# Kernel optimization log

Hardware: AMD Instinct MI355X
Metric: run time of the kernel (lower is better)

## Reference

```python
import jax, jax.numpy as jnp
import numpy as np


def setup_inputs() -> dict:
    key = jax.random.key(0)
    ks = jax.random.split(key, 8)
    bs, G, A, C, CM, D, H = 256, 169, 3, 5, 32, 1024, 512
    return {
        "boxes_sml0": jax.random.uniform(ks[0], (bs, G, A, C), dtype=jnp.float32),
        "masks_in0": jax.random.normal(ks[1], (bs, G, A, CM), dtype=jnp.float32),
        "feat": jax.random.normal(ks[2], (bs, D, 13, 13), dtype=jnp.float32),
        "lang_feat": jax.random.normal(ks[3], (bs, H), dtype=jnp.float32),
        "W_vs": jax.random.normal(ks[4], (D, H), dtype=jnp.float32) * 0.02,
        "b_vs": jnp.zeros((H,), dtype=jnp.float32),
        "W_ts": jax.random.normal(ks[5], (H, H), dtype=jnp.float32) * 0.02,
        "b_ts": jnp.zeros((H,), dtype=jnp.float32),
        "select_num": 32,
    }


def reference(boxes_sml0, masks_in0, feat, lang_feat, W_vs, b_vs, W_ts, b_ts, select_num):
    bs, G, A, C = boxes_sml0.shape
    CM = masks_in0.shape[-1]
    D = feat.shape[1]

    # mean over anchors of objectness channel 4 -> top-k grid selection
    mean_score = jnp.mean(boxes_sml0[..., 4], axis=2)           # [bs, G]
    _, idx = jax.lax.top_k(mean_score, select_num)              # [bs, k]

    # scatter-mask + masked_select in torch == gather of selected grids
    boxes_new = jnp.take_along_axis(boxes_sml0, idx[:, :, None, None], axis=1)  # [bs,k,A,C]
    masks_new = jnp.take_along_axis(masks_in0, idx[:, :, None, None], axis=1)   # [bs,k,A,CM]

    # gather visual features of selected grids, project
    i_all = feat.reshape(bs, D, -1).transpose(0, 2, 1)          # [bs, G, D]
    i_sel = jnp.take_along_axis(i_all, idx[:, :, None], axis=1) # [bs, k, D]
    x_new = i_sel @ W_vs + b_vs                                 # [bs, k, H]
    y_new = lang_feat @ W_ts + b_ts                             # [bs, H]

    # head: visual-text similarity, pick top grid per batch
    sim = jnp.einsum('bkh,bh->bk', x_new, y_new)                # [bs, k]
    maxval = jnp.max(sim, axis=1)                               # [bs]
    pred = jnp.argmax(sim, axis=1)                              # [bs]

    sel_b = jnp.take_along_axis(boxes_new, pred[:, None, None, None], axis=1)[:, 0]  # [bs,A,C]
    sel_m = jnp.take_along_axis(masks_new, pred[:, None, None, None], axis=1)[:, 0]  # [bs,A,CM]

    # cxcywh -> xyxy with original in-place overwrite semantics
    cx, cy, w, h = sel_b[..., 0], sel_b[..., 1], sel_b[..., 2], sel_b[..., 3]
    x1 = cx - w / 2
    y1 = cy - h / 2
    x2 = x1 + w
    y2 = y1 + h
    refined = jnp.concatenate(
        [jnp.stack([x1, y1, x2, y2], axis=-1), sel_b[..., 4:]], axis=-1)  # [bs,A,C]

    # pick anchor with max objectness, gather 5-dim box and mask coeffs
    aidx = jnp.argmax(refined[..., 4], axis=1)                  # [bs]
    box_new = jnp.take_along_axis(refined[..., :5], aidx[:, None, None], axis=1)  # [bs,1,5]
    mask_new = jnp.take_along_axis(sel_m, aidx[:, None, None], axis=1)            # [bs,1,CM]
    return box_new, mask_new, maxval
```

## Files before the change

### kernel.cpp

```cpp
#include <hip/hip_runtime.h>
#include <cfloat>
#include <cstdint>

#define GBM 64
#define GBN 64
#define GBK 64
#define GPAD 68

#define G_    169
#define D_    1024
#define NW    8
#define SLAB  128
#define ROWG  8
#define NGRP  16
#define GRPF  1352
#define NV    338
#define NBUF  3
#define SPL   8

typedef unsigned int u32;

__device__ __forceinline__ void gload_lds16(const float* g, float* l) {
    __builtin_amdgcn_global_load_lds(
        (const __attribute__((address_space(1))) u32*)g,
        (__attribute__((address_space(3))) u32*)l, 16, 0, 0);
}

__device__ __forceinline__ void stage_group(const float* gsrc, float* ldsbase, int lane) {
    #pragma unroll
    for (int j = 0; j < 6; j++) {
        int idx = j * 64 + lane;
        if (idx < NV)
            gload_lds16(gsrc + 4 * idx, ldsbase + j * 256);
    }
}

__global__ __launch_bounds__(256) void gemm_splitk(
    const float* __restrict__ A, const float* __restrict__ B,
    float* __restrict__ Cpart, int M, int N, int K)
{
    __shared__ __align__(16) float Asm[GBK][GPAD];
    __shared__ __align__(16) float Bsm[GBK][GPAD];
    int t  = threadIdx.x;
    int m0 = blockIdx.y * GBM, n0 = blockIdx.x * GBN;
    int ks = blockIdx.z * GBK;

    #pragma unroll
    for (int i = 0; i < 4; i++) {
        int v = t + 256 * i;
        int m = v >> 4, k4 = (v & 15) * 4;
        float4 x = *(const float4*)&A[(size_t)(m0 + m) * K + ks + k4];
        Asm[k4 + 0][m] = x.x; Asm[k4 + 1][m] = x.y;
        Asm[k4 + 2][m] = x.z; Asm[k4 + 3][m] = x.w;
    }
    #pragma unroll
    for (int i = 0; i < 4; i++) {
        int v = t + 256 * i;
        int r = v >> 4, c4 = (v & 15) * 4;
        *(float4*)&Bsm[r][c4] = *(const float4*)&B[(size_t)(ks + r) * N + n0 + c4];
    }
    __syncthreads();

    int r4 = (t >> 4) * 4, c4 = (t & 15) * 4;
    float acc[4][4] = {{0.f}};
    #pragma unroll
    for (int kk = 0; kk < GBK; kk++) {
        float4 a = *(const float4*)&Asm[kk][r4];
        float4 b = *(const float4*)&Bsm[kk][c4];
        float av[4] = {a.x, a.y, a.z, a.w};
        float bv[4] = {b.x, b.y, b.z, b.w};
        #pragma unroll
        for (int i = 0; i < 4; i++)
            #pragma unroll
            for (int j = 0; j < 4; j++) acc[i][j] += av[i] * bv[j];
    }
    float* Cp = Cpart + (size_t)blockIdx.z * M * N;
    #pragma unroll
    for (int i = 0; i < 4; i++) {
        float4 v = {acc[i][0], acc[i][1], acc[i][2], acc[i][3]};
        *(float4*)&Cp[(size_t)(m0 + r4 + i) * N + n0 + c4] = v;
    }
}

__global__ __launch_bounds__(256) void gemm2_fused(
    const float* __restrict__ py, const float* __restrict__ b_ts,
    const float* __restrict__ W, float* __restrict__ pz,
    int M, int N, int K)
{
    __shared__ __align__(16) float Asm[GBK][GPAD];
    __shared__ __align__(16) float Bsm[GBK][GPAD];
    int t  = threadIdx.x;
    int m0 = blockIdx.y * GBM, n0 = blockIdx.x * GBN;
    int ks = blockIdx.z * GBK;

    #pragma unroll
    for (int i = 0; i < 4; i++) {
        int v = t + 256 * i;
        int m = v >> 4, h4 = (v & 15) * 4;
        float4 x = *(const float4*)&b_ts[ks + h4];
        #pragma unroll
        for (int s = 0; s < SPL; s++) {
            float4 p = *(const float4*)&py[((size_t)s * M + m0 + m) * K + ks + h4];
            x.x += p.x; x.y += p.y; x.z += p.z; x.w += p.w;
        }
        Asm[h4 + 0][m] = x.x; Asm[h4 + 1][m] = x.y;
        Asm[h4 + 2][m] = x.z; Asm[h4 + 3][m] = x.w;
    }
    #pragma unroll
    for (int i = 0; i < 4; i++) {
        int v = t + 256 * i;
        int n = v >> 4, k4 = (v & 15) * 4;
        float4 x = *(const float4*)&W[(size_t)(n0 + n) * K + ks + k4];
        Bsm[k4 + 0][n] = x.x; Bsm[k4 + 1][n] = x.y;
        Bsm[k4 + 2][n] = x.z; Bsm[k4 + 3][n] = x.w;
    }
    __syncthreads();

    int r4 = (t >> 4) * 4, c4 = (t & 15) * 4;
    float acc[4][4] = {{0.f}};
    #pragma unroll
    for (int kk = 0; kk < GBK; kk++) {
        float4 a = *(const float4*)&Asm[kk][r4];
        float4 b = *(const float4*)&Bsm[kk][c4];
        float av[4] = {a.x, a.y, a.z, a.w};
        float bv[4] = {b.x, b.y, b.z, b.w};
        #pragma unroll
        for (int i = 0; i < 4; i++)
            #pragma unroll
            for (int j = 0; j < 4; j++) acc[i][j] += av[i] * bv[j];
    }
    float* Cp = pz + (size_t)blockIdx.z * M * N;
    #pragma unroll
    for (int i = 0; i < 4; i++) {
        float4 v = {acc[i][0], acc[i][1], acc[i][2], acc[i][3]};
        *(float4*)&Cp[(size_t)(m0 + r4 + i) * N + n0 + c4] = v;
    }
}

__global__ __launch_bounds__(512) void feat_final(
    const float* __restrict__ feat, const float* __restrict__ pz,
    const float* __restrict__ boxes, const float* __restrict__ masks,
    const float* __restrict__ py, const float* __restrict__ b_ts,
    const float* __restrict__ b_vs, const int* __restrict__ kptr,
    float* __restrict__ out_box, float* __restrict__ out_mask,
    float* __restrict__ out_max,
    int bs, int AN, int CH, int CM, int H)
{
    __shared__ __align__(16) float buf[NW][NBUF][GRPF];
    __shared__ __align__(16) float zs[D_];
    __shared__ float accw[NW * 192];
    __shared__ float simall[176];
    __shared__ float ms[176];
    __shared__ int   selg[176];
    __shared__ float simv[176];
    __shared__ float redw[NW];
    __shared__ float bbs;
    __shared__ int   selp[2];

    const int b = blockIdx.x;
    const int t = threadIdx.x;
    const int w = t >> 6, lane = t & 63;

    {
        int h2 = t * 2;
        float2 s = {0.f, 0.f};
        #pragma unroll
        for (int sp = 0; sp < SPL; sp++) {
            float2 v = *(const float2*)&pz[((size_t)sp * bs + b) * D_ + h2];
            s.x += v.x; s.y += v.y;
        }
        *(float2*)&zs[h2] = s;
    }
    __syncthreads();

    const float* gsrc = feat + ((size_t)b * D_ + (size_t)w * SLAB) * G_;
    stage_group(gsrc,        buf[w][0], lane);
    stage_group(gsrc + GRPF, buf[w][1], lane);

    float acc0 = 0.f, acc1 = 0.f, acc2 = 0.f;
    const bool g2 = lane < (G_ - 128);
    for (int gi = 0; gi < NGRP; gi++) {
        if (gi + 2 < NGRP) {
            stage_group(gsrc + (size_t)(gi + 2) * GRPF, buf[w][(gi + 2) % NBUF], lane);
            asm volatile("s_waitcnt vmcnt(12)" ::: "memory");
        } else if (gi + 1 < NGRP) {
            asm volatile("s_waitcnt vmcnt(6)" ::: "memory");
        } else {
            asm volatile("s_waitcnt vmcnt(0)" ::: "memory");
        }
        __builtin_amdgcn_sched_barrier(0);
        const float* bp = buf[w][gi % NBUF];
        const float* zp = &zs[w * SLAB + gi * ROWG];
        #pragma unroll
        for (int r = 0; r < ROWG; r++) {
            float zv = zp[r];
            acc0 += bp[r * G_ + lane] * zv;
            acc1 += bp[r * G_ + lane + 64] * zv;
            if (g2) acc2 += bp[r * G_ + lane + 128] * zv;
        }
    }
    accw[w * 192 + lane]       = acc0;
    accw[w * 192 + lane + 64]  = acc1;
    if (g2) accw[w * 192 + lane + 128] = acc2;
    __syncthreads();

    int k = *kptr; if (k > G_) k = G_;

    if (t < G_) {
        float s = 0.f;
        #pragma unroll
        for (int ww = 0; ww < NW; ww++) s += accw[ww * 192 + t];
        simall[t] = s;
        const float* bp = boxes + (size_t)(b * G_ + t) * AN * CH;
        float o = 0.f;
        for (int a = 0; a < AN; a++) o += bp[a * CH + 4];
        ms[t] = o / (float)AN;
    }
    {
        float part = 0.f;
        for (int h = t; h < H; h += 512) {
            float yv = b_ts[h];
            #pragma unroll
            for (int s = 0; s < SPL; s++) yv += py[((size_t)s * bs + b) * H + h];
            part += b_vs[h] * yv;
        }
        #pragma unroll
        for (int off = 32; off > 0; off >>= 1) part += __shfl_down(part, off);
        if (lane == 0) redw[w] = part;
    }
    __syncthreads();
    if (t == 0) {
        float s = 0.f;
        #pragma unroll
        for (int ww = 0; ww < NW; ww++) s += redw[ww];
        bbs = s;
    }

    if (t < G_) {
        float mv = ms[t];
        int rank = 0;
        for (int g = 0; g < G_; g++) {
            float o = ms[g];
            rank += (int)((o > mv) | ((o == mv) & (g < t)));
        }
        if (rank < k) selg[rank] = t;
    }
    __syncthreads();

    if (t < k) simv[t] = simall[selg[t]];
    __syncthreads();

    if (t == 0) {
        float best = -FLT_MAX; int br = 0;
        for (int r = 0; r < k; r++) if (simv[r] > best) { best = simv[r]; br = r; }
        int gs = selg[br];
        const float* bp = boxes + (size_t)(b * G_ + gs) * AN * CH;
        float bo = -FLT_MAX; int ai = 0;
        for (int a = 0; a < AN; a++) { float o = bp[a * CH + 4]; if (o > bo) { bo = o; ai = a; } }
        float cx = bp[ai * CH + 0], cy = bp[ai * CH + 1];
        float ww = bp[ai * CH + 2], hh = bp[ai * CH + 3];
        float x1 = cx - ww * 0.5f, y1 = cy - hh * 0.5f;
        out_box[(size_t)b * CH + 0] = x1;
        out_box[(size_t)b * CH + 1] = y1;
        out_box[(size_t)b * CH + 2] = x1 + ww;
        out_box[(size_t)b * CH + 3] = y1 + hh;
        for (int c = 4; c < CH; c++) out_box[(size_t)b * CH + c] = bp[ai * CH + c];
        out_max[b] = best + bbs;
        selp[0] = gs; selp[1] = ai;
    }
    __syncthreads();
    if (t < CM) {
        out_mask[(size_t)b * CM + t] =
            masks[((size_t)(b * G_ + selp[0]) * AN + selp[1]) * CM + t];
    }
}

extern "C" void kernel_launch(void* const* d_in, const int* in_sizes, int n_in,
                              void* d_out, int out_size, void* d_ws, size_t ws_size,
                              hipStream_t stream)
{
    const float* boxes = (const float*)d_in[0];
    const float* masks = (const float*)d_in[1];
    const float* feat  = (const float*)d_in[2];
    const float* lang  = (const float*)d_in[3];
    const float* W_vs  = (const float*)d_in[4];
    const float* b_vs  = (const float*)d_in[5];
    const float* W_ts  = (const float*)d_in[6];
    const float* b_ts  = (const float*)d_in[7];
    const int*   kptr  = (const int*)d_in[8];

    int H  = in_sizes[5];
    int D  = in_sizes[4] / H;
    int bs = in_sizes[3] / H;
    int AN = 3;
    int CH = in_sizes[0] / (bs * G_ * AN);
    int CM = in_sizes[1] / (bs * G_ * AN);

    float* py = (float*)d_ws;
    float* pz = py + (size_t)SPL * bs * H;

    float* out_box  = (float*)d_out;
    float* out_mask = out_box + (size_t)bs * CH;
    float* out_max  = out_mask + (size_t)bs * CM;

    dim3 g1(H / GBN, bs / GBM, SPL);
    gemm_splitk<<<g1, 256, 0, stream>>>(lang, W_ts, py, bs, H, H);
    dim3 g2(D / GBN, bs / GBM, SPL);
    gemm2_fused<<<g2, 256, 0, stream>>>(py, b_ts, W_vs, pz, bs, D, H);
    feat_final<<<bs, 512, 0, stream>>>(feat, pz, boxes, masks, py, b_ts, b_vs,
                                       kptr, out_box, out_mask, out_max,
                                       bs, AN, CH, CM, H);
}
```

Baseline: 57.68 us.

## Fuse W_vs projection into feat kernel with producer/consumer warp specialization

```diff
diff --git a/kernel.cpp b/kernel.cpp
--- a/kernel.cpp
+++ b/kernel.cpp
@@ -9,10 +9,10 @@
 
 #define G_    169
 #define D_    1024
-#define NW    8
-#define SLAB  128
+#define H_    512
+#define NSW   6
+#define NCHUNK 128
 #define ROWG  8
-#define NGRP  16
 #define GRPF  1352
 #define NV    338
 #define NBUF  3
@@ -82,78 +82,26 @@
     }
 }
 
-__global__ __launch_bounds__(256) void gemm2_fused(
-    const float* __restrict__ py, const float* __restrict__ b_ts,
-    const float* __restrict__ W, float* __restrict__ pz,
-    int M, int N, int K)
-{
-    __shared__ __align__(16) float Asm[GBK][GPAD];
-    __shared__ __align__(16) float Bsm[GBK][GPAD];
-    int t  = threadIdx.x;
-    int m0 = blockIdx.y * GBM, n0 = blockIdx.x * GBN;
-    int ks = blockIdx.z * GBK;
-
-    #pragma unroll
-    for (int i = 0; i < 4; i++) {
-        int v = t + 256 * i;
-        int m = v >> 4, h4 = (v & 15) * 4;
-        float4 x = *(const float4*)&b_ts[ks + h4];
-        #pragma unroll
-        for (int s = 0; s < SPL; s++) {
-            float4 p = *(const float4*)&py[((size_t)s * M + m0 + m) * K + ks + h4];
-            x.x += p.x; x.y += p.y; x.z += p.z; x.w += p.w;
-        }
-        Asm[h4 + 0][m] = x.x; Asm[h4 + 1][m] = x.y;
-        Asm[h4 + 2][m] = x.z; Asm[h4 + 3][m] = x.w;
-    }
-    #pragma unroll
-    for (int i = 0; i < 4; i++) {
-        int v = t + 256 * i;
-        int n = v >> 4, k4 = (v & 15) * 4;
-        float4 x = *(const float4*)&W[(size_t)(n0 + n) * K + ks + k4];
-        Bsm[k4 + 0][n] = x.x; Bsm[k4 + 1][n] = x.y;
-        Bsm[k4 + 2][n] = x.z; Bsm[k4 + 3][n] = x.w;
-    }
-    __syncthreads();
-
-    int r4 = (t >> 4) * 4, c4 = (t & 15) * 4;
-    float acc[4][4] = {{0.f}};
-    #pragma unroll
-    for (int kk = 0; kk < GBK; kk++) {
-        float4 a = *(const float4*)&Asm[kk][r4];
-        float4 b = *(const float4*)&Bsm[kk][c4];
-        float av[4] = {a.x, a.y, a.z, a.w};
-        float bv[4] = {b.x, b.y, b.z, b.w};
-        #pragma unroll
-        for (int i = 0; i < 4; i++)
-            #pragma unroll
-            for (int j = 0; j < 4; j++) acc[i][j] += av[i] * bv[j];
-    }
-    float* Cp = pz + (size_t)blockIdx.z * M * N;
-    #pragma unroll
-    for (int i = 0; i < 4; i++) {
-        float4 v = {acc[i][0], acc[i][1], acc[i][2], acc[i][3]};
-        *(float4*)&Cp[(size_t)(m0 + r4 + i) * N + n0 + c4] = v;
-    }
-}
-
 __global__ __launch_bounds__(512) void feat_final(
-    const float* __restrict__ feat, const float* __restrict__ pz,
+    const float* __restrict__ feat, const float* __restrict__ py,
+    const float* __restrict__ W_vs,
     const float* __restrict__ boxes, const float* __restrict__ masks,
-    const float* __restrict__ py, const float* __restrict__ b_ts,
-    const float* __restrict__ b_vs, const int* __restrict__ kptr,
+    const float* __restrict__ b_ts, const float* __restrict__ b_vs,
+    const int* __restrict__ kptr,
     float* __restrict__ out_box, float* __restrict__ out_mask,
     float* __restrict__ out_max,
-    int bs, int AN, int CH, int CM, int H)
+    int bs, int AN, int CH, int CM)
 {
-    __shared__ __align__(16) float buf[NW][NBUF][GRPF];
+    __shared__ __align__(16) float buf[NSW][NBUF][GRPF];
     __shared__ __align__(16) float zs[D_];
-    __shared__ float accw[NW * 192];
-    __shared__ float simall[176];
+    __shared__ __align__(16) float ycopy[2][H_];
+    __shared__ float accw[NSW * 176];
+    __shared__ int   zp[2];
     __shared__ float ms[176];
     __shared__ int   selg[176];
     __shared__ float simv[176];
-    __shared__ float redw[NW];
+    __shared__ float simall[176];
+    __shared__ float redw[8];
     __shared__ float bbs;
     __shared__ int   selp[2];
 
@@ -161,47 +109,87 @@
     const int t = threadIdx.x;
     const int w = t >> 6, lane = t & 63;
 
-    {
-        int h2 = t * 2;
-        float2 s = {0.f, 0.f};
-        #pragma unroll
-        for (int sp = 0; sp < SPL; sp++) {
-            float2 v = *(const float2*)&pz[((size_t)sp * bs + b) * D_ + h2];
-            s.x += v.x; s.y += v.y;
-        }
-        *(float2*)&zs[h2] = s;
-    }
-    __syncthreads();
-
-    const float* gsrc = feat + ((size_t)b * D_ + (size_t)w * SLAB) * G_;
-    stage_group(gsrc,        buf[w][0], lane);
-    stage_group(gsrc + GRPF, buf[w][1], lane);
-
-    float acc0 = 0.f, acc1 = 0.f, acc2 = 0.f;
-    const bool g2 = lane < (G_ - 128);
-    for (int gi = 0; gi < NGRP; gi++) {
-        if (gi + 2 < NGRP) {
-            stage_group(gsrc + (size_t)(gi + 2) * GRPF, buf[w][(gi + 2) % NBUF], lane);
-            asm volatile("s_waitcnt vmcnt(12)" ::: "memory");
-        } else if (gi + 1 < NGRP) {
-            asm volatile("s_waitcnt vmcnt(6)" ::: "memory");
-        } else {
-            asm volatile("s_waitcnt vmcnt(0)" ::: "memory");
-        }
-        __builtin_amdgcn_sched_barrier(0);
-        const float* bp = buf[w][gi % NBUF];
-        const float* zp = &zs[w * SLAB + gi * ROWG];
-        #pragma unroll
-        for (int r = 0; r < ROWG; r++) {
-            float zv = zp[r];
-            acc0 += bp[r * G_ + lane] * zv;
-            acc1 += bp[r * G_ + lane + 64] * zv;
-            if (g2) acc2 += bp[r * G_ + lane + 128] * zv;
-        }
-    }
-    accw[w * 192 + lane]       = acc0;
-    accw[w * 192 + lane + 64]  = acc1;
-    if (g2) accw[w * 192 + lane + 128] = acc2;
+    if (t == 0) { zp[0] = 0; zp[1] = 0; }
+    __syncthreads();
+
+    if (w >= NSW) {
+        const int pw = w - NSW;
+        {
+            int l4 = lane * 4;
+            float4 s0 = *(const float4*)&b_ts[l4];
+            float4 s1 = *(const float4*)&b_ts[256 + l4];
+            #pragma unroll
+            for (int s = 0; s < SPL; s++) {
+                const float* pyb = &py[((size_t)s * bs + b) * H_];
+                float4 a0 = *(const float4*)&pyb[l4];
+                float4 a1 = *(const float4*)&pyb[256 + l4];
+                s0.x += a0.x; s0.y += a0.y; s0.z += a0.z; s0.w += a0.w;
+                s1.x += a1.x; s1.y += a1.y; s1.z += a1.z; s1.w += a1.w;
+            }
+            *(float4*)&ycopy[pw][l4] = s0;
+            *(float4*)&ycopy[pw][256 + l4] = s1;
+        }
+        asm volatile("s_waitcnt lgkmcnt(0)" ::: "memory");
+        float4 yv[16];
+        {
+            const float* yb = &ycopy[pw][(lane & 7) * 64];
+            #pragma unroll
+            for (int j = 0; j < 16; j++) yv[j] = *(const float4*)&yb[4 * j];
+        }
+        const int myrow = lane >> 3;
+        for (int i = 0; i < NCHUNK / 2; i++) {
+            int c = 2 * i + pw;
+            const float* wr = &W_vs[(size_t)(8 * c + myrow) * H_ + (lane & 7) * 64];
+            float part = 0.f;
+            #pragma unroll
+            for (int j = 0; j < 16; j++) {
+                float4 v = *(const float4*)&wr[4 * j];
+                part += v.x * yv[j].x + v.y * yv[j].y + v.z * yv[j].z + v.w * yv[j].w;
+            }
+            part += __shfl_xor(part, 1);
+            part += __shfl_xor(part, 2);
+            part += __shfl_xor(part, 4);
+            if ((lane & 7) == 0) zs[8 * c + myrow] = part;
+            asm volatile("s_waitcnt lgkmcnt(0)" ::: "memory");
+            if (lane == 0) ((volatile int*)zp)[pw] = i + 1;
+        }
+    } else {
+        const int n = (NCHUNK - 1 - w) / NSW + 1;
+        const float* gsrc = feat + (size_t)b * D_ * G_;
+        stage_group(gsrc + (size_t)w * GRPF,           buf[w][0], lane);
+        stage_group(gsrc + (size_t)(w + NSW) * GRPF,   buf[w][1], lane);
+
+        float acc0 = 0.f, acc1 = 0.f, acc2 = 0.f;
+        const bool g2 = lane < (G_ - 128);
+        for (int i = 0; i < n; i++) {
+            const int g = w + NSW * i;
+            if (i + 2 < n)
+                stage_group(gsrc + (size_t)(w + NSW * (i + 2)) * GRPF,
+                            buf[w][(i + 2) % NBUF], lane);
+            {
+                int par = g & 1, need = (g >> 1) + 1;
+                while (((volatile int*)zp)[par] < need)
+                    __builtin_amdgcn_s_sleep(2);
+            }
+            asm volatile("s_waitcnt lgkmcnt(0)" ::: "memory");
+            if (i + 2 < n)      asm volatile("s_waitcnt vmcnt(12)" ::: "memory");
+            else if (i + 1 < n) asm volatile("s_waitcnt vmcnt(6)"  ::: "memory");
+            else                asm volatile("s_waitcnt vmcnt(0)"  ::: "memory");
+            __builtin_amdgcn_sched_barrier(0);
+            const float* bp = buf[w][i % NBUF];
+            const float* zpv = &zs[8 * g];
+            #pragma unroll
+            for (int r = 0; r < ROWG; r++) {
+                float zv = zpv[r];
+                acc0 += bp[r * G_ + lane] * zv;
+                acc1 += bp[r * G_ + lane + 64] * zv;
+                if (g2) acc2 += bp[r * G_ + lane + 128] * zv;
+            }
+        }
+        accw[w * 176 + lane]      = acc0;
+        accw[w * 176 + lane + 64] = acc1;
+        if (g2) accw[w * 176 + lane + 128] = acc2;
+    }
     __syncthreads();
 
     int k = *kptr; if (k > G_) k = G_;
@@ -209,7 +197,7 @@
     if (t < G_) {
         float s = 0.f;
         #pragma unroll
-        for (int ww = 0; ww < NW; ww++) s += accw[ww * 192 + t];
+        for (int ww = 0; ww < NSW; ww++) s += accw[ww * 176 + t];
         simall[t] = s;
         const float* bp = boxes + (size_t)(b * G_ + t) * AN * CH;
         float o = 0.f;
@@ -217,13 +205,7 @@
         ms[t] = o / (float)AN;
     }
     {
-        float part = 0.f;
-        for (int h = t; h < H; h += 512) {
-            float yv = b_ts[h];
-            #pragma unroll
-            for (int s = 0; s < SPL; s++) yv += py[((size_t)s * bs + b) * H + h];
-            part += b_vs[h] * yv;
-        }
+        float part = b_vs[t] * ycopy[0][t];
         #pragma unroll
         for (int off = 32; off > 0; off >>= 1) part += __shfl_down(part, off);
         if (lane == 0) redw[w] = part;
@@ -232,7 +214,7 @@
     if (t == 0) {
         float s = 0.f;
         #pragma unroll
-        for (int ww = 0; ww < NW; ww++) s += redw[ww];
+        for (int ww = 0; ww < 8; ww++) s += redw[ww];
         bbs = s;
     }
 
@@ -290,14 +272,12 @@
     const int*   kptr  = (const int*)d_in[8];
 
     int H  = in_sizes[5];
-    int D  = in_sizes[4] / H;
     int bs = in_sizes[3] / H;
     int AN = 3;
     int CH = in_sizes[0] / (bs * G_ * AN);
     int CM = in_sizes[1] / (bs * G_ * AN);
 
     float* py = (float*)d_ws;
-    float* pz = py + (size_t)SPL * bs * H;
 
     float* out_box  = (float*)d_out;
     float* out_mask = out_box + (size_t)bs * CH;
@@ -305,9 +285,7 @@
 
     dim3 g1(H / GBN, bs / GBM, SPL);
     gemm_splitk<<<g1, 256, 0, stream>>>(lang, W_ts, py, bs, H, H);
-    dim3 g2(D / GBN, bs / GBM, SPL);
-    gemm2_fused<<<g2, 256, 0, stream>>>(py, b_ts, W_vs, pz, bs, D, H);
-    feat_final<<<bs, 512, 0, stream>>>(feat, pz, boxes, masks, py, b_ts, b_vs,
+    feat_final<<<bs, 512, 0, stream>>>(feat, py, W_vs, boxes, masks, b_ts, b_vs,
                                        kptr, out_box, out_mask, out_max,
-                                       bs, AN, CH, CM, H);
-}
+                                       bs, AN, CH, CM);
+}
```

Result: slower. 90.06 us (+56.1%).
